# Performance work log

Measured on AMD Instinct MI355X. Metric: run time of the kernel, lower is better.

The kernel has to match this reference:

```python
import jax, jax.numpy as jnp
import numpy as np

B, C, H, W = 64, 256, 14, 14
K = 9
HID = 256   # EdgeAgg hidden_channels = in_channels
OUT = 512   # out_channels = 2*in_channels (required by final reshape)


def _knn(q, kset, k):
    # ViG dense_knn_matrix: squared-distance knn, top-k of -dist (self-loop may be included)
    qs = jnp.sum(q * q, -1)
    ks = jnp.sum(kset * kset, -1)
    dist = qs[:, :, None] - 2.0 * jnp.einsum('bnc,bmc->bnm', q, kset) + ks[:, None, :]
    _, idx = jax.lax.top_k(-dist, k)   # (B,N,k) neighbor indices into kset
    return idx


def _edgeconv_add(feat, nbr, validf, w, b):
    # PyG EdgeConv(nn=Linear, aggr='add') with per-node valid-edge mask:
    #   out[i] = sum_{j in valid nbrs(i)} cat(x_i, x_j - x_i) @ w + b
    # nn is linear, so aggregate neighbor diffs BEFORE the matmul (same math, less traffic).
    Cf = feat.shape[-1]
    wa, wb = w[:Cf], w[Cf:]
    deg = jnp.sum(validf, -1, keepdims=True)                   # (B,N,1)
    xj = feat[jnp.arange(feat.shape[0])[:, None, None], nbr]   # (B,N,k,C) gather
    sum_xj = jnp.einsum('bnkc,bnk->bnc', xj, validf)
    return deg * (feat @ wa + b) + (sum_xj - deg * feat) @ wb


def _forward(x, fc1_w, fc1_b, fc2_w, fc2_b, fce_w, fce_b, inout_w, inout_b,
             attn_w, attn_b, upd_w, upd_b, kp_w, kp_b, enc_w, enc_b,
             mu_w, mu_b, dec_w, dec_b, T):
    k = dec_w.shape[-1]
    b_, c_, h_, w_ = x.shape
    n = h_ * w_
    xs = x.reshape(b_, c_, n)                       # (B,C,N)
    x_sp = jnp.transpose(xs, (0, 2, 1))             # (B,N,C) true spatial node feats for knn
    x_sp_d = jax.lax.stop_gradient(x_sp)            # original detaches before knn
    x_nbr = _knn(x_sp_d, x_sp_d, k)
    # temporal roll across the T frames of each clip
    y_sp = jnp.roll(x_sp.reshape(b_ // T, T, n, c_), -1, axis=1).reshape(b_, n, c_)
    y_nbr = _knn(x_sp_d, jax.lax.stop_gradient(y_sp), k)
    # faithful to original: x.view(B*N, C) reinterprets the contiguous (B,C,N) buffer
    x_feat = xs.reshape(b_, n, c_)
    y_feat = jnp.transpose(y_sp, (0, 2, 1)).reshape(b_, n, c_)
    # VAE-like K predictor (deterministic z = mu); argmax -> per-node degree in [0,k)
    hk = x_feat.reshape(b_ * n, c_) @ kp_w + kp_b
    hk = jax.nn.relu(hk @ enc_w + enc_b)
    mu = hk @ mu_w + mu_b
    logits = mu @ dec_w + dec_b                     # (B*N, k)
    k_int = jnp.argmax(logits, axis=1)
    # generate_mask: keep the first k_int[i] of node i's k edges
    validf = (jnp.arange(k)[None, :] < k_int[:, None]).astype(x.dtype).reshape(b_, n, k)

    def edge_agg(feat, nbr):
        h1 = jax.nn.relu(_edgeconv_add(feat, nbr, validf, fc1_w, fc1_b))
        h2 = _edgeconv_add(h1, nbr, validf, fc2_w, fc2_b)
        return (h2 @ fce_w + fce_b).reshape(b_ * n, -1)

    x_agg = edge_agg(x_feat, x_nbr)
    y_agg = edge_agg(y_feat, y_nbr)
    scores = (jnp.concatenate([x_agg, y_agg], -1) @ attn_w + attn_b)[:, 0]
    wgt = jax.nn.softmax(scores, axis=0)[:, None]   # softmax over ALL B*N nodes (as in source)
    fused = wgt * x_agg + (1.0 - wgt) * y_agg
    xin = x_feat.reshape(b_ * n, c_) @ inout_w + inout_b
    upd = jax.nn.relu(jnp.concatenate([xin, fused], -1) @ upd_w + upd_b)   # (B*N, 2C)
    return jnp.transpose(upd.reshape(b_, n, 2 * c_), (0, 2, 1)).reshape(b_, 2 * c_, h_, w_)


def setup_inputs():
    key = jax.random.key(0)
    ks = iter(jax.random.split(key, 32))

    def lin(i, o):
        return jax.random.normal(next(ks), (i, o), jnp.float32) / np.sqrt(i)

    def bias(o):
        return jax.random.normal(next(ks), (o,), jnp.float32) * 0.01

    return {
        'x': jax.random.normal(next(ks), (B, C, H, W), jnp.float32),
        'fc1_w': lin(2 * C, HID), 'fc1_b': bias(HID),
        'fc2_w': lin(2 * HID, HID), 'fc2_b': bias(HID),
        'fce_w': lin(HID, OUT), 'fce_b': bias(OUT),
        'inout_w': lin(C, OUT), 'inout_b': bias(OUT),
        'attn_w': lin(2 * OUT, 1), 'attn_b': bias(1),
        'upd_w': lin(2 * OUT, OUT), 'upd_b': bias(OUT),
        'kp_w': lin(C, 500), 'kp_b': bias(500),
        'enc_w': lin(500, 64), 'enc_b': bias(64),
        'mu_w': lin(64, 32), 'mu_b': bias(32),
        'dec_w': lin(32, K), 'dec_b': bias(K),
        'T': 16,
    }


def reference(x, fc1_w, fc1_b, fc2_w, fc2_b, fce_w, fce_b, inout_w, inout_b,
              attn_w, attn_b, upd_w, upd_b, kp_w, kp_b, enc_w, enc_b,
              mu_w, mu_b, dec_w, dec_b, T):
    return _forward(x, fc1_w, fc1_b, fc2_w, fc2_b, fce_w, fce_b, inout_w, inout_b,
                    attn_w, attn_b, upd_w, upd_b, kp_w, kp_b, enc_w, enc_b,
                    mu_w, mu_b, dec_w, dec_b, T)
```

## Files before the change

### kernel.cpp

```cpp
#include <hip/hip_runtime.h>
#include <cstddef>
#include <cstdint>

constexpr int BATCH = 64;
constexpr int CH    = 256;
constexpr int NPT   = 196;
constexpr int ROWS  = BATCH * NPT;
constexpr int BSTRIDE = CH * NPT;
constexpr int KNB   = 8;
constexpr int DSTR  = 208;

typedef __bf16 bf16x8 __attribute__((ext_vector_type(8)));
typedef __bf16 bf16x4 __attribute__((ext_vector_type(4)));
typedef _Float16 f16x8 __attribute__((ext_vector_type(8)));
typedef float  f32x4  __attribute__((ext_vector_type(4)));
typedef unsigned long long u64;

__device__ __forceinline__ int src_batch(int b) {
    return (b & ~15) | ((b + 1) & 15);
}

__device__ __forceinline__ void gload_lds16(const void* g, void* l) {
    __builtin_amdgcn_global_load_lds(
        (const __attribute__((address_space(1))) void*)g,
        (__attribute__((address_space(3))) void*)l, 16, 0, 0);
}

__device__ __forceinline__ int xcd_swz(int lin, int nwg) {
    int q = nwg >> 3;
    return (lin & 7) * q + (lin >> 3);
}

__global__ __launch_bounds__(256) void front_kernel(const float* __restrict__ x,
        _Float16* __restrict__ XH, _Float16* __restrict__ XL,
        __bf16* __restrict__ XB, float* __restrict__ qsp,
        const float* __restrict__ fc1_w, const float* __restrict__ fc2_w,
        const float* __restrict__ fce_w, const float* __restrict__ upd_w,
        const float* __restrict__ kp_w, const float* __restrict__ kp_b,
        const float* __restrict__ enc_w, const float* __restrict__ enc_b,
        const float* __restrict__ mu_w, const float* __restrict__ mu_b,
        const float* __restrict__ dec_w, const float* __restrict__ dec_b,
        const float* __restrict__ inout_w, const float* __restrict__ inout_b,
        const float* __restrict__ upd_b,
        __bf16* __restrict__ W1catT, __bf16* __restrict__ W2catT,
        __bf16* __restrict__ fcet, __bf16* __restrict__ updC,
        float* __restrict__ KW1, float* __restrict__ kb1,
        float* __restrict__ KW2, float* __restrict__ kb2,
        float* __restrict__ bcomp, int* __restrict__ smcnt) {
    __shared__ __attribute__((aligned(16))) char smem[16896];
    float (*tile)[65] = (float(*)[65])smem;
    int bid = blockIdx.x;
    int t = threadIdx.x;
    if (bid < 1024) {
        int m0 = (bid & 3) * 64, c0 = ((bid >> 2) & 3) * 64, b = bid >> 4;
        const float* xb = x + (size_t)b * BSTRIDE;
        #pragma unroll
        for (int s = 0; s < 16; ++s) {
            int idx = s * 256 + t;
            int cc = idx >> 6, mm = idx & 63;
            int m = m0 + mm;
            float v = (m < NPT) ? xb[(size_t)(c0 + cc) * NPT + m] : 0.f;
            tile[cc][mm] = v;
            if (m < NPT)
                XB[(size_t)b * BSTRIDE + (size_t)(c0 + cc) * NPT + m] = (__bf16)v;
        }
        __syncthreads();
        #pragma unroll
        for (int s = 0; s < 16; ++s) {
            int idx = s * 256 + t;
            int mm = idx >> 6, cc = idx & 63;
            float v = tile[cc][mm];
            _Float16 h = (_Float16)v;
            size_t off = ((size_t)b * 256 + (m0 + mm)) * 256 + c0 + cc;
            XH[off] = h;
            XL[off] = (_Float16)(v - (float)h);
        }
        if (t < 64) {
            float acc = 0.f;
            #pragma unroll
            for (int cc = 0; cc < 64; ++cc) {
                float v = tile[cc][t];
                acc = fmaf(v, v, acc);
            }
            qsp[(size_t)(c0 >> 6) * 16384 + b * 256 + m0 + t] = acc;
        }
    } else {
        int pbid = bid - 1024;
        if (pbid == 0 && t == 0) smcnt[0] = 0;
        if (pbid < 64) {
            const float* W = (pbid < 32) ? fc1_w : fc2_w;
            __bf16* WT = (pbid < 32) ? W1catT : W2catT;
            int local = pbid & 31;
            int n0 = (local >> 2) * 64, k0 = (local & 3) * 64;
            #pragma unroll
            for (int s = 0; s < 16; ++s) {
                int idx = s * 256 + t;
                int kk = idx >> 6, nn = idx & 63;
                float v;
                if (n0 < 256)
                    v = W[(size_t)(k0 + kk) * 256 + n0 + nn] -
                        W[(size_t)(k0 + kk + 256) * 256 + n0 + nn];
                else
                    v = W[(size_t)(k0 + kk + 256) * 256 + (n0 - 256) + nn];
                tile[kk][nn] = v;
            }
            __syncthreads();
            #pragma unroll
            for (int s = 0; s < 16; ++s) {
                int idx = s * 256 + t;
                int nn = idx >> 6, kk = idx & 63;
                WT[(size_t)(n0 + nn) * 256 + k0 + kk] = (__bf16)tile[kk][nn];
            }
        } else if (pbid < 96) {
            int local = pbid - 64;
            int n0 = (local >> 2) * 64, k0 = (local & 3) * 64;
            #pragma unroll
            for (int s = 0; s < 16; ++s) {
                int idx = s * 256 + t;
                int kk = idx >> 6, nn = idx & 63;
                tile[kk][nn] = fce_w[(size_t)(k0 + kk) * 512 + n0 + nn];
            }
            __syncthreads();
            #pragma unroll
            for (int s = 0; s < 16; ++s) {
                int idx = s * 256 + t;
                int nn = idx >> 6, kk = idx & 63;
                fcet[(size_t)(n0 + nn) * 256 + k0 + kk] = (__bf16)tile[kk][nn];
            }
        } else if (pbid < 160) {
            int local = pbid - 96;
            int k0 = (local >> 3) * 64, n0 = (local & 7) * 64;
            #pragma unroll
            for (int s = 0; s < 16; ++s) {
                int idx = s * 256 + t;
                int kk = idx >> 6, nn = idx & 63;
                tile[kk][nn] = upd_w[(size_t)(512 + k0 + kk) * 512 + n0 + nn];
            }
            __syncthreads();
            #pragma unroll
            for (int s = 0; s < 16; ++s) {
                int idx = s * 256 + t;
                int nn = idx >> 6, kk = idx & 63;
                updC[(size_t)(n0 + nn) * 768 + 256 + k0 + kk] = (__bf16)tile[kk][nn];
            }
        } else if (pbid < 224) {
            int i = (pbid - 160) * 4 + (t >> 6);
            int j = t & 63;
            double acc = 0.0;
            for (int k = 0; k < 500; ++k)
                acc += (double)kp_w[(size_t)i * 500 + k] * (double)enc_w[(size_t)k * 64 + j];
            KW1[i * 64 + j] = (float)acc;
        } else if (pbid == 224) {
            int j = t;
            if (j < 64) {
                double acc = (double)enc_b[j];
                for (int k = 0; k < 500; ++k)
                    acc += (double)kp_b[k] * (double)enc_w[(size_t)k * 64 + j];
                kb1[j] = (float)acc;
            }
        } else if (pbid < 228) {
            int e = (pbid - 225) * 256 + t;
            if (e < 576) {
                int i = e / 9, j = e - (e / 9) * 9;
                double acc = 0.0;
                for (int k = 0; k < 32; ++k)
                    acc += (double)mu_w[(size_t)i * 32 + k] * (double)dec_w[(size_t)k * 9 + j];
                KW2[e] = (float)acc;
            } else if (e < 585) {
                int j = e - 576;
                double acc = (double)dec_b[j];
                for (int k = 0; k < 32; ++k)
                    acc += (double)mu_b[k] * (double)dec_w[(size_t)k * 9 + j];
                kb2[j] = (float)acc;
            }
        } else if (pbid < 740) {
            int e = (pbid - 228) * 256 + t;
            int k = e >> 9, n = e & 511;
            double acc = 0.0;
            for (int j = 0; j < 512; ++j)
                acc += (double)inout_w[(size_t)k * 512 + j] * (double)upd_w[(size_t)j * 512 + n];
            updC[(size_t)n * 768 + k] = (__bf16)(float)acc;
        } else {
            int n = (pbid - 740) * 256 + t;
            double acc = (double)upd_b[n];
            for (int j = 0; j < 512; ++j)
                acc += (double)inout_b[j] * (double)upd_w[(size_t)j * 512 + n];
            bcomp[n] = (float)acc;
        }
    }
}

__global__ __launch_bounds__(256) void gram_kint(const _Float16* __restrict__ XH,
        const _Float16* __restrict__ XL, const float* __restrict__ qsp,
        float* __restrict__ Dw, const float* __restrict__ x,
        const float* __restrict__ W1, const float* __restrict__ b1,
        const float* __restrict__ W2, const float* __restrict__ b2,
        int* __restrict__ kint, float* __restrict__ degf) {
    __shared__ __attribute__((aligned(16))) char smem[32768];
    int bid = blockIdx.x;
    int t = threadIdx.x;
    if (bid < 2048) {
        int nid = xcd_swz(bid, 2048);
        int job = nid >> 4;
        int tile = nid & 15;
        int by = tile >> 2, bx = tile & 3;
        int r0 = by * 64, c0 = bx * 64;
        int qb = (job < 64) ? job : job - 64;
        int kb = (job < 64) ? qb : src_batch(qb);
        int w = t >> 6, l = t & 63;
        int lr = l & 15, lg = l >> 4;
        int wr = (w >> 1) * 32, wc = (w & 1) * 32;
        const _Float16* qh = XH + (size_t)qb * 65536;
        const _Float16* ql = XL + (size_t)qb * 65536;
        const _Float16* kh = XH + (size_t)kb * 65536;
        const _Float16* kl = XL + (size_t)kb * 65536;
        int srow = w * 16 + (l >> 2);
        int scb = (l & 3) * 8;
        f32x4 acc[2][2] = {};
        auto stage = [&](int k0, int bsel) {
            _Float16* base = (_Float16*)(smem + bsel * 16384);
            size_t goA = (size_t)(r0 + srow) * 256 + k0 + scb;
            size_t goB = (size_t)(c0 + srow) * 256 + k0 + scb;
            gload_lds16(qh + goA, base + w * 512);
            gload_lds16(ql + goA, base + 2048 + w * 512);
            gload_lds16(kh + goB, base + 4096 + w * 512);
            gload_lds16(kl + goB, base + 6144 + w * 512);
        };
        stage(0, 0);
        #pragma unroll
        for (int ks8 = 0; ks8 < 8; ++ks8) {
            if (ks8 < 7) {
                stage((ks8 + 1) * 32, (ks8 + 1) & 1);
                asm volatile("s_waitcnt vmcnt(4)" ::: "memory");
            } else {
                asm volatile("s_waitcnt vmcnt(0)" ::: "memory");
            }
            __syncthreads();
            _Float16* base = (_Float16*)(smem + (ks8 & 1) * 16384);
            _Float16* Ah = base;
            _Float16* Al = base + 2048;
            _Float16* Bh = base + 4096;
            _Float16* Bl = base + 6144;
            f16x8 ah[2], alv[2], bh[2], blv[2];
            #pragma unroll
            for (int mi = 0; mi < 2; ++mi) {
                ah[mi]  = *(const f16x8*)(Ah + (wr + mi * 16 + lr) * 32 + lg * 8);
                alv[mi] = *(const f16x8*)(Al + (wr + mi * 16 + lr) * 32 + lg * 8);
            }
            #pragma unroll
            for (int ni = 0; ni < 2; ++ni) {
                bh[ni]  = *(const f16x8*)(Bh + (wc + ni * 16 + lr) * 32 + lg * 8);
                blv[ni] = *(const f16x8*)(Bl + (wc + ni * 16 + lr) * 32 + lg * 8);
            }
            #pragma unroll
            for (int mi = 0; mi < 2; ++mi)
                #pragma unroll
                for (int ni = 0; ni < 2; ++ni) {
                    acc[mi][ni] = __builtin_amdgcn_mfma_f32_16x16x32_f16(
                        ah[mi], bh[ni], acc[mi][ni], 0, 0, 0);
                    acc[mi][ni] = __builtin_amdgcn_mfma_f32_16x16x32_f16(
                        ah[mi], blv[ni], acc[mi][ni], 0, 0, 0);
                    acc[mi][ni] = __builtin_amdgcn_mfma_f32_16x16x32_f16(
                        alv[mi], bh[ni], acc[mi][ni], 0, 0, 0);
                }
            __syncthreads();
        }
        float ksv[2];
        #pragma unroll
        for (int ni = 0; ni < 2; ++ni) {
            int col = c0 + wc + ni * 16 + lr;
            if (col < NPT) {
                size_t o0 = (size_t)kb * 256 + col;
                ksv[ni] = ((qsp[o0] + qsp[16384 + o0]) + qsp[32768 + o0]) +
                          qsp[49152 + o0];
            } else ksv[ni] = 0.f;
        }
        #pragma unroll
        for (int mi = 0; mi < 2; ++mi) {
            #pragma unroll
            for (int r = 0; r < 4; ++r) {
                if (r0 + wr + mi * 16 + r >= NPT) continue;
                int grow = r0 + wr + mi * 16 + lg * 4 + r;
                if (grow >= NPT) continue;
                size_t o0 = (size_t)qb * 256 + grow;
                float qq = ((qsp[o0] + qsp[16384 + o0]) + qsp[32768 + o0]) +
                           qsp[49152 + o0];
                size_t rbase = ((size_t)job * NPT + grow) * DSTR;
                #pragma unroll
                for (int ni = 0; ni < 2; ++ni) {
                    int col = c0 + wc + ni * 16 + lr;
                    if (col < NPT)
                        Dw[rbase + col] = qq - 2.f * acc[mi][ni][r] + ksv[ni];
                }
            }
        }
    } else {
        float (*xr)[256] = (float(*)[256])smem;
        float (*ebuf)[64] = (float(*)[64])(smem + 16384);
        float (*lg2)[9]  = (float(*)[9])(smem + 20480);
        int r0 = (bid - 2048) * 16;
        const float4* xg = (const float4*)(x + (size_t)r0 * 256);
        float4* xs = (float4*)&xr[0][0];
        #pragma unroll
        for (int s = 0; s < 4; ++s) xs[s * 256 + t] = xg[s * 256 + t];
        __syncthreads();
        int w = t >> 6, l = t & 63;
        {
            float bb = b1[l];
            float a0 = bb, a1 = bb, a2 = bb, a3 = bb;
            const float* x0 = xr[w * 4 + 0];
            const float* x1 = xr[w * 4 + 1];
            const float* x2 = xr[w * 4 + 2];
            const float* x3 = xr[w * 4 + 3];
            for (int c = 0; c < 256; ++c) {
                float wv = W1[c * 64 + l];
                a0 = fmaf(x0[c], wv, a0);
                a1 = fmaf(x1[c], wv, a1);
                a2 = fmaf(x2[c], wv, a2);
                a3 = fmaf(x3[c], wv, a3);
            }
            ebuf[w * 4 + 0][l] = fmaxf(a0, 0.f);
            ebuf[w * 4 + 1][l] = fmaxf(a1, 0.f);
            ebuf[w * 4 + 2][l] = fmaxf(a2, 0.f);
            ebuf[w * 4 + 3][l] = fmaxf(a3, 0.f);
        }
        __syncthreads();
        int rr = t >> 4, cc = t & 15;
        if (cc < 9) {
            float acc = b2[cc];
            for (int j = 0; j < 64; ++j)
                acc = fmaf(ebuf[rr][j], W2[j * 9 + cc], acc);
            lg2[rr][cc] = acc;
        }
        __syncthreads();
        if (cc == 0) {
            float best = lg2[rr][0];
            int bi = 0;
            #pragma unroll
            for (int j = 1; j < 9; ++j)
                if (lg2[rr][j] > best) { best = lg2[rr][j]; bi = j; }
            kint[r0 + rr] = bi;
            degf[r0 + rr] = (float)bi;
        }
    }
}

__global__ __launch_bounds__(256) void topk_p1(const float* __restrict__ Dw,
        int* __restrict__ nbr, const __bf16* __restrict__ XB,
        const __bf16* __restrict__ W1catT, __bf16* __restrict__ P1) {
    __shared__ __attribute__((aligned(16))) char smem[32768];
    int bid = blockIdx.x;
    int t = threadIdx.x;
    if (bid < 392) {
        u64 (*lists)[4][8] = (u64(*)[4][8])smem;
        int lrow = t >> 2, q = t & 3;
        int rowid = bid * 64 + lrow;
        const float* rp = Dw + (size_t)rowid * DSTR + q * 52;
        u64 kreg[8];
        #pragma unroll
        for (int p = 0; p < 8; ++p) kreg[p] = ~0ull;
        for (int s4 = 0; s4 < 13; ++s4) {
            f32x4 dv = *(const f32x4*)(rp + s4 * 4);
            #pragma unroll
            for (int e = 0; e < 4; ++e) {
                int col = q * 52 + s4 * 4 + e;
                unsigned u = __float_as_uint(dv[e]);
                u = (u & 0x80000000u) ? ~u : (u | 0x80000000u);
                u64 key = (col < NPT) ? (((u64)u << 32) | (unsigned)col) : ~0ull;
                if (key < kreg[7]) {
                    #pragma unroll
                    for (int p = 0; p < 8; ++p) {
                        u64 mn = (key < kreg[p]) ? key : kreg[p];
                        u64 mx = (key < kreg[p]) ? kreg[p] : key;
                        kreg[p] = mn; key = mx;
                    }
                }
            }
        }
        #pragma unroll
        for (int p = 0; p < 8; ++p) lists[lrow][q][p] = kreg[p];
        __syncthreads();
        if (q == 0) {
            const u64* c = &lists[lrow][0][0];
            int p0 = 0, p1 = 0, p2 = 0, p3 = 0;
            #pragma unroll
            for (int it = 0; it < 8; ++it) {
                u64 v0 = c[p0], v1 = c[8 + p1], v2 = c[16 + p2], v3 = c[24 + p3];
                u64 best = v0; int bj = 0;
                if (v1 < best) { best = v1; bj = 1; }
                if (v2 < best) { best = v2; bj = 2; }
                if (v3 < best) { best = v3; bj = 3; }
                if (bj == 0) p0 = (p0 < 7) ? p0 + 1 : 7;
                else if (bj == 1) p1 = (p1 < 7) ? p1 + 1 : 7;
                else if (bj == 2) p2 = (p2 < 7) ? p2 + 1 : 7;
                else p3 = (p3 < 7) ? p3 + 1 : 7;
                nbr[(size_t)rowid * KNB + it] = (int)(best & 0xffffffffu);
            }
        }
    } else {
        __bf16* As = (__bf16*)smem;
        __bf16* Bs = As + 128 * 64;
        int lin = bid - 392;
        int nid = xcd_swz(lin, 392);
        int bx = nid & 3, by = nid >> 2;
        int w = t >> 6, l = t & 63;
        int r0 = by * 128, c0 = bx * 128;
        int lr = l & 15, lg = l >> 4;
        int wr = (w >> 1) * 64, wc = (w & 1) * 64;
        constexpr int K = 256, N = 512;
        f32x4 acc[4][4] = {};
        for (int k0 = 0; k0 < K; k0 += 64) {
            #pragma unroll
            for (int i = 0; i < 4; ++i) {
                int row = (w * 4 + i) * 8 + (l >> 3);
                int c8 = l & 7;
                gload_lds16(XB + (size_t)(r0 + row) * K + k0 + c8 * 8,
                            As + (w * 4 + i) * 512);
                gload_lds16(W1catT + (size_t)(c0 + row) * K + k0 + c8 * 8,
                            Bs + (w * 4 + i) * 512);
            }
            asm volatile("s_waitcnt vmcnt(0)" ::: "memory");
            __syncthreads();
            #pragma unroll
            for (int ks = 0; ks < 2; ++ks) {
                bf16x8 af[4], bfr[4];
                #pragma unroll
                for (int mi = 0; mi < 4; ++mi)
                    af[mi] = *(const bf16x8*)(As + (wr + mi * 16 + lr) * 64 + ks * 32 + lg * 8);
                #pragma unroll
                for (int ni = 0; ni < 4; ++ni)
                    bfr[ni] = *(const bf16x8*)(Bs + (wc + ni * 16 + lr) * 64 + ks * 32 + lg * 8);
                #pragma unroll
                for (int mi = 0; mi < 4; ++mi)
                    #pragma unroll
                    for (int ni = 0; ni < 4; ++ni)
                        acc[mi][ni] = __builtin_amdgcn_mfma_f32_16x16x32_bf16(
                            af[mi], bfr[ni], acc[mi][ni], 0, 0, 0);
            }
            __syncthreads();
        }
        #pragma unroll
        for (int mi = 0; mi < 4; ++mi) {
            #pragma unroll
            for (int r = 0; r < 4; ++r) {
                int row = r0 + wr + mi * 16 + lg * 4 + r;
                #pragma unroll
                for (int ni = 0; ni < 4; ++ni) {
                    int col = c0 + wc + ni * 16 + lr;
                    P1[(size_t)row * N + col] = (__bf16)acc[mi][ni][r];
                }
            }
        }
    }
}

template<int STAGE, int RELU>
__global__ __launch_bounds__(256) void combine_kernel(const __bf16* __restrict__ P,
        const int* __restrict__ nbr, const int* __restrict__ kint_,
        const float* __restrict__ degf, const float* __restrict__ bias,
        __bf16* __restrict__ H) {
    int g = threadIdx.x >> 6, lane = threadIdx.x & 63;
    int nid = xcd_swz(blockIdx.x, 2 * ROWS / 4);
    int r = nid * 4 + g;
    int branch = (r >= ROWS);
    int rr = r - branch * ROWS;
    int b = rr / NPT, i = rr - b * NPT;
    size_t srow, mbase;
    if constexpr (STAGE == 1) {
        int fb = branch ? src_batch(b) : b;
        srow = (size_t)fb * NPT + i;
        mbase = (size_t)fb * NPT;
    } else {
        srow = (size_t)r;
        mbase = (size_t)branch * ROWS + (size_t)b * NPT;
    }
    const int* nb = nbr + (size_t)branch * ((size_t)ROWS * KNB) + (size_t)rr * KNB;
    bf16x4 sv = *(const bf16x4*)(P + srow * 512 + lane * 4);
    float4 bv = *(const float4*)(bias + lane * 4);
    float s0 = 0.f, s1 = 0.f, s2 = 0.f, s3 = 0.f;
    int kk = kint_[rr];
    for (int tt = 0; tt < kk; ++tt) {
        int m = nb[tt];
        bf16x4 v = *(const bf16x4*)(P + (mbase + m) * 512 + 256 + lane * 4);
        s0 += (float)v[0]; s1 += (float)v[1]; s2 += (float)v[2]; s3 += (float)v[3];
    }
    float dg = degf[rr];
    float o0 = fmaf(dg, (float)sv[0] + bv.x, s0);
    float o1 = fmaf(dg, (float)sv[1] + bv.y, s1);
    float o2 = fmaf(dg, (float)sv[2] + bv.z, s2);
    float o3 = fmaf(dg, (float)sv[3] + bv.w, s3);
    if constexpr (RELU) {
        o0 = fmaxf(o0, 0.f); o1 = fmaxf(o1, 0.f);
        o2 = fmaxf(o2, 0.f); o3 = fmaxf(o3, 0.f);
    }
    bf16x4 ov;
    ov[0] = (__bf16)o0; ov[1] = (__bf16)o1; ov[2] = (__bf16)o2; ov[3] = (__bf16)o3;
    *(bf16x4*)(H + (size_t)r * 256 + lane * 4) = ov;
}

template<int FLAGS, int CONCAT>
__global__ __launch_bounds__(256) void mfma_gemm(
    const __bf16* __restrict__ A0, const __bf16* __restrict__ A1,
    const __bf16* __restrict__ WT, const float* __restrict__ bias,
    float* __restrict__ Cf, __bf16* __restrict__ Cb, int K, int N,
    const float* __restrict__ aw, float* __restrict__ scp,
    const float* __restrict__ wgt) {
    constexpr int SMEMB = (FLAGS & 8) ? (128 * 129 * 4) : (2 * 128 * 64 * 2);
    __shared__ __attribute__((aligned(16))) char smem[SMEMB];
    __bf16* As = (__bf16*)smem;
    __bf16* Bs = As + 128 * 64;
    int lin = blockIdx.x + 4 * blockIdx.y;
    int nid = xcd_swz(lin, 4 * gridDim.y);
    int bx = nid & 3, by = nid >> 2;
    int t = threadIdx.x, w = t >> 6, l = t & 63;
    int r0 = by * 128, c0 = bx * 128;
    int lr = l & 15, lg = l >> 4;
    int wr = (w >> 1) * 64, wc = (w & 1) * 64;
    f32x4 acc[4][4] = {};
    for (int k0 = 0; k0 < K; k0 += 64) {
        #pragma unroll
        for (int i = 0; i < 4; ++i) {
            int row = (w * 4 + i) * 8 + (l >> 3);
            int c8 = l & 7;
            if constexpr (CONCAT == 2) {
                if (k0 < 256) {
                    gload_lds16(A0 + (size_t)(r0 + row) * 256 + k0 + c8 * 8,
                                As + (w * 4 + i) * 512);
                } else {
                    int kk2 = k0 - 256 + c8 * 8;
                    size_t gr = (size_t)(r0 + row);
                    bf16x8 xa = *(const bf16x8*)(A1 + gr * 512 + kk2);
                    bf16x8 ya = *(const bf16x8*)(A1 + ((size_t)ROWS + gr) * 512 + kk2);
                    float wv = wgt[gr];
                    bf16x8 mx;
                    #pragma unroll
                    for (int j = 0; j < 8; ++j)
                        mx[j] = (__bf16)(wv * (float)xa[j] + (1.f - wv) * (float)ya[j]);
                    *(bf16x8*)(As + (w * 4 + i) * 512 + l * 8) = mx;
                }
            } else {
                gload_lds16(A0 + (size_t)(r0 + row) * K + k0 + c8 * 8,
                            As + (w * 4 + i) * 512);
            }
            gload_lds16(WT + (size_t)(c0 + row) * K + k0 + c8 * 8,
                        Bs + (w * 4 + i) * 512);
        }
        asm volatile("s_waitcnt vmcnt(0)" ::: "memory");
        __syncthreads();
        #pragma unroll
        for (int ks = 0; ks < 2; ++ks) {
            bf16x8 af[4], bfr[4];
            #pragma unroll
            for (int mi = 0; mi < 4; ++mi)
                af[mi] = *(const bf16x8*)(As + (wr + mi * 16 + lr) * 64 + ks * 32 + lg * 8);
            #pragma unroll
            for (int ni = 0; ni < 4; ++ni)
                bfr[ni] = *(const bf16x8*)(Bs + (wc + ni * 16 + lr) * 64 + ks * 32 + lg * 8);
            #pragma unroll
            for (int mi = 0; mi < 4; ++mi)
                #pragma unroll
                for (int ni = 0; ni < 4; ++ni)
                    acc[mi][ni] = __builtin_amdgcn_mfma_f32_16x16x32_bf16(
                        af[mi], bfr[ni], acc[mi][ni], 0, 0, 0);
        }
        __syncthreads();
    }
    if constexpr ((FLAGS & 8) != 0) {
        float* tile = (float*)smem;
        #pragma unroll
        for (int mi = 0; mi < 4; ++mi)
            #pragma unroll
            for (int r = 0; r < 4; ++r) {
                int rrow = wr + mi * 16 + lg * 4 + r;
                #pragma unroll
                for (int ni = 0; ni < 4; ++ni) {
                    int ccol = wc + ni * 16 + lr;
                    float v = acc[mi][ni][r];
                    if (bias) v += bias[c0 + ccol];
                    if constexpr ((FLAGS & 1) != 0) v = fmaxf(v, 0.f);
                    tile[rrow * 129 + ccol] = v;
                }
            }
        __syncthreads();
        int cc = t >> 6, rr2 = t & 63;
        #pragma unroll
        for (int cs = 0; cs < 128; cs += 4) {
            #pragma unroll
            for (int h = 0; h < 2; ++h) {
                int row = r0 + rr2 + h * 64;
                int bb = row / NPT, ii = row - bb * NPT;
                Cf[((size_t)bb * 512 + (c0 + cc + cs)) * NPT + ii] =
                    tile[(rr2 + h * 64) * 129 + cc + cs];
            }
        }
    } else if constexpr ((FLAGS & 16) != 0) {
        int half = (r0 >= ROWS) ? 1 : 0;
        float ps[4][4] = {};
        #pragma unroll
        for (int mi = 0; mi < 4; ++mi)
            #pragma unroll
            for (int r = 0; r < 4; ++r) {
                int row = r0 + wr + mi * 16 + lg * 4 + r;
                #pragma unroll
                for (int ni = 0; ni < 4; ++ni) {
                    int col = c0 + wc + ni * 16 + lr;
                    float v = acc[mi][ni][r] + bias[col];
                    Cb[(size_t)row * N + col] = (__bf16)v;
                    ps[mi][r] = fmaf(v, aw[half * 512 + col], ps[mi][r]);
                }
            }
        #pragma unroll
        for (int m = 1; m <= 8; m <<= 1)
            #pragma unroll
            for (int mi = 0; mi < 4; ++mi)
                #pragma unroll
                for (int r = 0; r < 4; ++r)
                    ps[mi][r] += __shfl_xor(ps[mi][r], m, 64);
        if (lr == 0) {
            int slot = half * 8 + bx * 2 + (w & 1);
            #pragma unroll
            for (int mi = 0; mi < 4; ++mi)
                #pragma unroll
                for (int r = 0; r < 4; ++r) {
                    int sr = r0 - half * ROWS + wr + mi * 16 + lg * 4 + r;
                    scp[(size_t)slot * ROWS + sr] = ps[mi][r];
                }
        }
    } else {
        #pragma unroll
        for (int mi = 0; mi < 4; ++mi) {
            #pragma unroll
            for (int r = 0; r < 4; ++r) {
                int row = r0 + wr + mi * 16 + lg * 4 + r;
                #pragma unroll
                for (int ni = 0; ni < 4; ++ni) {
                    int col = c0 + wc + ni * 16 + lr;
                    float v = acc[mi][ni][r];
                    if (bias) v += bias[col];
                    if constexpr ((FLAGS & 1) != 0) v = fmaxf(v, 0.f);
                    if constexpr ((FLAGS & 4) != 0)
                        Cb[(size_t)row * N + col] = (__bf16)v;
                    else
                        Cf[(size_t)row * N + col] = v;
                }
            }
        }
    }
}

__global__ __launch_bounds__(256) void softmax_all(const float* __restrict__ scp,
        const float* __restrict__ ab, float* __restrict__ scores,
        float* __restrict__ mpart, float* __restrict__ spart,
        int* __restrict__ cnt, float* __restrict__ wgt) {
    __shared__ float red[256];
    __shared__ float MS[2];
    __shared__ bool islast;
    int t = threadIdx.x;
    int sr = blockIdx.x * 256 + t;
    float s = ab[0];
    #pragma unroll
    for (int i = 0; i < 16; ++i) s += scp[(size_t)i * ROWS + sr];
    scores[sr] = s;
    red[t] = s; __syncthreads();
    for (int off = 128; off; off >>= 1) {
        if (t < off) red[t] = fmaxf(red[t], red[t + off]);
        __syncthreads();
    }
    float mb = red[0]; __syncthreads();
    red[t] = expf(s - mb); __syncthreads();
    for (int off = 128; off; off >>= 1) {
        if (t < off) red[t] += red[t + off];
        __syncthreads();
    }
    if (t == 0) {
        mpart[blockIdx.x] = mb;
        spart[blockIdx.x] = red[0];
        __threadfence();
        int old = atomicAdd(cnt, 1);
        islast = (old == 48);
    }
    __syncthreads();
    if (!islast) return;
    __threadfence();
    if (t == 0) {
        float M = mpart[0];
        for (int i = 1; i < 49; ++i) M = fmaxf(M, mpart[i]);
        float S = 0.f;
        for (int i = 0; i < 49; ++i) S += spart[i] * expf(mpart[i] - M);
        MS[0] = M; MS[1] = S;
        cnt[0] = 0;
    }
    __syncthreads();
    float M = MS[0], denom = MS[1];
    for (int i = t; i < ROWS; i += 256)
        wgt[i] = expf(scores[i] - M) / denom;
}

extern "C" void kernel_launch(void* const* d_in, const int* in_sizes, int n_in,
                              void* d_out, int out_size, void* d_ws, size_t ws_size,
                              hipStream_t stream) {
    (void)in_sizes; (void)n_in; (void)out_size; (void)ws_size;
    const float* x       = (const float*)d_in[0];
    const float* fc1_w   = (const float*)d_in[1];
    const float* fc1_b   = (const float*)d_in[2];
    const float* fc2_w   = (const float*)d_in[3];
    const float* fc2_b   = (const float*)d_in[4];
    const float* fce_w   = (const float*)d_in[5];
    const float* fce_b   = (const float*)d_in[6];
    const float* inout_w = (const float*)d_in[7];
    const float* inout_b = (const float*)d_in[8];
    const float* attn_w  = (const float*)d_in[9];
    const float* attn_b  = (const float*)d_in[10];
    const float* upd_w   = (const float*)d_in[11];
    const float* upd_b   = (const float*)d_in[12];
    const float* kp_w    = (const float*)d_in[13];
    const float* kp_b    = (const float*)d_in[14];
    const float* enc_w   = (const float*)d_in[15];
    const float* enc_b   = (const float*)d_in[16];
    const float* mu_w    = (const float*)d_in[17];
    const float* mu_b    = (const float*)d_in[18];
    const float* dec_w   = (const float*)d_in[19];
    const float* dec_b   = (const float*)d_in[20];
    float* out = (float*)d_out;

    char* base = (char*)d_ws;
    size_t o = 0;
    auto alloc = [&](size_t bytes) -> void* {
        void* p = base + o;
        o += (bytes + 255) & ~(size_t)255;
        return p;
    };
    float* qsp    = (float*)alloc((size_t)4 * 64 * 256 * 4);
    float* degf   = (float*)alloc(ROWS * 4);
    float* scores = (float*)alloc(ROWS * 4);
    float* wgt    = (float*)alloc(ROWS * 4);
    int*   kint   = (int*)  alloc(ROWS * 4);
    float* KW1    = (float*)alloc(256 * 64 * 4);
    float* kb1    = (float*)alloc(64 * 4);
    float* KW2    = (float*)alloc(64 * 9 * 4);
    float* kb2    = (float*)alloc(9 * 4);
    float* bcomp  = (float*)alloc(512 * 4);
    float* scp    = (float*)alloc((size_t)16 * ROWS * 4);
    float* mpart  = (float*)alloc(64 * 4);
    float* spart  = (float*)alloc(64 * 4);
    int*   smcnt  = (int*)  alloc(256);
    int*   nbr    = (int*)  alloc((size_t)128 * NPT * KNB * 4);
    char*  regD   = (char*) alloc((size_t)ROWS * 512 * 2);
    __bf16* XB    = (__bf16*)alloc((size_t)ROWS * 256 * 2);
    __bf16* H1    = (__bf16*)alloc((size_t)2 * ROWS * 256 * 2);
    __bf16* H2    = (__bf16*)alloc((size_t)2 * ROWS * 256 * 2);
    char*  regAGG = (char*) alloc((size_t)2 * ROWS * 512 * 4);
    __bf16* W1catT= (__bf16*)alloc((size_t)512 * 256 * 2);
    __bf16* W2catT= (__bf16*)alloc((size_t)512 * 256 * 2);
    __bf16* fcet  = (__bf16*)alloc((size_t)512 * 256 * 2);
    __bf16* updC  = (__bf16*)alloc((size_t)512 * 768 * 2);
    __bf16* P1buf = (__bf16*)regD;
    _Float16* XSPH = (_Float16*)regAGG;
    _Float16* XSPL = XSPH + (size_t)64 * 256 * 256;
    float* Dw     = (float*)(regAGG + (size_t)17 * 1024 * 1024);
    __bf16* P2buf = (__bf16*)regAGG;
    __bf16* AGGb  = (__bf16*)regAGG;
    __bf16* XAGGb = AGGb;

    front_kernel<<<1766, 256, 0, stream>>>(x, XSPH, XSPL, XB, qsp,
                                           fc1_w, fc2_w, fce_w, upd_w,
                                           kp_w, kp_b, enc_w, enc_b,
                                           mu_w, mu_b, dec_w, dec_b,
                                           inout_w, inout_b, upd_b,
                                           W1catT, W2catT, fcet, updC,
                                           KW1, kb1, KW2, kb2, bcomp, smcnt);

    gram_kint<<<2832, 256, 0, stream>>>(XSPH, XSPL, qsp, Dw, x,
                                        KW1, kb1, KW2, kb2, kint, degf);

    topk_p1<<<784, 256, 0, stream>>>(Dw, nbr, XB, W1catT, P1buf);

    combine_kernel<1, 1><<<2 * ROWS / 4, 256, 0, stream>>>(
        P1buf, nbr, kint, degf, fc1_b, H1);

    mfma_gemm<4, 0><<<dim3(4, 196), 256, 0, stream>>>(
        H1, nullptr, W2catT, nullptr, nullptr, P2buf, 256, 512,
        nullptr, nullptr, nullptr);
    combine_kernel<2, 0><<<2 * ROWS / 4, 256, 0, stream>>>(
        P2buf, nbr, kint, degf, fc2_b, H2);

    mfma_gemm<20, 0><<<dim3(4, 196), 256, 0, stream>>>(
        H2, nullptr, fcet, fce_b, nullptr, AGGb, 256, 512,
        attn_w, scp, nullptr);

    softmax_all<<<49, 256, 0, stream>>>(scp, attn_b, scores, mpart, spart,
                                        smcnt, wgt);

    mfma_gemm<9, 2><<<dim3(4, 98), 256, 0, stream>>>(
        XB, XAGGb, updC, bcomp, out, nullptr, 768, 512,
        nullptr, nullptr, wgt);
}
```

Baseline: 210.7 us.

## Move later-stage weight prep from front kernel into topk kernel blocks

The fc2, fce and upd weight transposes, the fp64 inout·upd weight fold and the bias fold now run as extra blocks of the top-k/P1 kernel instead of the front kernel. Only the fc1 transpose and the K-predictor weight folds stay in the front kernel. This shortens the front kernel, which sits on the critical path before the gram kernel, and lets the weight prep overlap with top-k work whose results are not needed until later stages. In exchange the top-k launch grows and its tail may lengthen, especially from the slow fp64 512-length dot-product blocks.

```diff
diff --git a/kernel.cpp b/kernel.cpp
--- a/kernel.cpp
+++ b/kernel.cpp
@@ -34,19 +34,15 @@
 __global__ __launch_bounds__(256) void front_kernel(const float* __restrict__ x,
         _Float16* __restrict__ XH, _Float16* __restrict__ XL,
         __bf16* __restrict__ XB, float* __restrict__ qsp,
-        const float* __restrict__ fc1_w, const float* __restrict__ fc2_w,
-        const float* __restrict__ fce_w, const float* __restrict__ upd_w,
+        const float* __restrict__ fc1_w,
         const float* __restrict__ kp_w, const float* __restrict__ kp_b,
         const float* __restrict__ enc_w, const float* __restrict__ enc_b,
         const float* __restrict__ mu_w, const float* __restrict__ mu_b,
         const float* __restrict__ dec_w, const float* __restrict__ dec_b,
-        const float* __restrict__ inout_w, const float* __restrict__ inout_b,
-        const float* __restrict__ upd_b,
-        __bf16* __restrict__ W1catT, __bf16* __restrict__ W2catT,
-        __bf16* __restrict__ fcet, __bf16* __restrict__ updC,
+        __bf16* __restrict__ W1catT,
         float* __restrict__ KW1, float* __restrict__ kb1,
         float* __restrict__ KW2, float* __restrict__ kb2,
-        float* __restrict__ bcomp, int* __restrict__ smcnt) {
+        int* __restrict__ smcnt) {
     __shared__ __attribute__((aligned(16))) char smem[16896];
     float (*tile)[65] = (float(*)[65])smem;
     int bid = blockIdx.x;
@@ -84,73 +80,17 @@
             }
             qsp[(size_t)(c0 >> 6) * 16384 + b * 256 + m0 + t] = acc;
         }
-    } else {
+    } else if (bid < 1092) {
         int pbid = bid - 1024;
         if (pbid == 0 && t == 0) smcnt[0] = 0;
         if (pbid < 64) {
-            const float* W = (pbid < 32) ? fc1_w : fc2_w;
-            __bf16* WT = (pbid < 32) ? W1catT : W2catT;
-            int local = pbid & 31;
-            int n0 = (local >> 2) * 64, k0 = (local & 3) * 64;
-            #pragma unroll
-            for (int s = 0; s < 16; ++s) {
-                int idx = s * 256 + t;
-                int kk = idx >> 6, nn = idx & 63;
-                float v;
-                if (n0 < 256)
-                    v = W[(size_t)(k0 + kk) * 256 + n0 + nn] -
-                        W[(size_t)(k0 + kk + 256) * 256 + n0 + nn];
-                else
-                    v = W[(size_t)(k0 + kk + 256) * 256 + (n0 - 256) + nn];
-                tile[kk][nn] = v;
-            }
-            __syncthreads();
-            #pragma unroll
-            for (int s = 0; s < 16; ++s) {
-                int idx = s * 256 + t;
-                int nn = idx >> 6, kk = idx & 63;
-                WT[(size_t)(n0 + nn) * 256 + k0 + kk] = (__bf16)tile[kk][nn];
-            }
-        } else if (pbid < 96) {
-            int local = pbid - 64;
-            int n0 = (local >> 2) * 64, k0 = (local & 3) * 64;
-            #pragma unroll
-            for (int s = 0; s < 16; ++s) {
-                int idx = s * 256 + t;
-                int kk = idx >> 6, nn = idx & 63;
-                tile[kk][nn] = fce_w[(size_t)(k0 + kk) * 512 + n0 + nn];
-            }
-            __syncthreads();
-            #pragma unroll
-            for (int s = 0; s < 16; ++s) {
-                int idx = s * 256 + t;
-                int nn = idx >> 6, kk = idx & 63;
-                fcet[(size_t)(n0 + nn) * 256 + k0 + kk] = (__bf16)tile[kk][nn];
-            }
-        } else if (pbid < 160) {
-            int local = pbid - 96;
-            int k0 = (local >> 3) * 64, n0 = (local & 7) * 64;
-            #pragma unroll
-            for (int s = 0; s < 16; ++s) {
-                int idx = s * 256 + t;
-                int kk = idx >> 6, nn = idx & 63;
-                tile[kk][nn] = upd_w[(size_t)(512 + k0 + kk) * 512 + n0 + nn];
-            }
-            __syncthreads();
-            #pragma unroll
-            for (int s = 0; s < 16; ++s) {
-                int idx = s * 256 + t;
-                int nn = idx >> 6, kk = idx & 63;
-                updC[(size_t)(n0 + nn) * 768 + 256 + k0 + kk] = (__bf16)tile[kk][nn];
-            }
-        } else if (pbid < 224) {
-            int i = (pbid - 160) * 4 + (t >> 6);
+            int i = pbid * 4 + (t >> 6);
             int j = t & 63;
             double acc = 0.0;
             for (int k = 0; k < 500; ++k)
                 acc += (double)kp_w[(size_t)i * 500 + k] * (double)enc_w[(size_t)k * 64 + j];
             KW1[i * 64 + j] = (float)acc;
-        } else if (pbid == 224) {
+        } else if (pbid == 64) {
             int j = t;
             if (j < 64) {
                 double acc = (double)enc_b[j];
@@ -158,8 +98,8 @@
                     acc += (double)kp_b[k] * (double)enc_w[(size_t)k * 64 + j];
                 kb1[j] = (float)acc;
             }
-        } else if (pbid < 228) {
-            int e = (pbid - 225) * 256 + t;
+        } else {
+            int e = (pbid - 65) * 256 + t;
             if (e < 576) {
                 int i = e / 9, j = e - (e / 9) * 9;
                 double acc = 0.0;
@@ -173,19 +113,28 @@
                     acc += (double)mu_b[k] * (double)dec_w[(size_t)k * 9 + j];
                 kb2[j] = (float)acc;
             }
-        } else if (pbid < 740) {
-            int e = (pbid - 228) * 256 + t;
-            int k = e >> 9, n = e & 511;
-            double acc = 0.0;
-            for (int j = 0; j < 512; ++j)
-                acc += (double)inout_w[(size_t)k * 512 + j] * (double)upd_w[(size_t)j * 512 + n];
-            updC[(size_t)n * 768 + k] = (__bf16)(float)acc;
-        } else {
-            int n = (pbid - 740) * 256 + t;
-            double acc = (double)upd_b[n];
-            for (int j = 0; j < 512; ++j)
-                acc += (double)inout_b[j] * (double)upd_w[(size_t)j * 512 + n];
-            bcomp[n] = (float)acc;
+        }
+    } else {
+        int local = bid - 1092;
+        int n0 = (local >> 2) * 64, k0 = (local & 3) * 64;
+        #pragma unroll
+        for (int s = 0; s < 16; ++s) {
+            int idx = s * 256 + t;
+            int kk = idx >> 6, nn = idx & 63;
+            float v;
+            if (n0 < 256)
+                v = fc1_w[(size_t)(k0 + kk) * 256 + n0 + nn] -
+                    fc1_w[(size_t)(k0 + kk + 256) * 256 + n0 + nn];
+            else
+                v = fc1_w[(size_t)(k0 + kk + 256) * 256 + (n0 - 256) + nn];
+            tile[kk][nn] = v;
+        }
+        __syncthreads();
+        #pragma unroll
+        for (int s = 0; s < 16; ++s) {
+            int idx = s * 256 + t;
+            int nn = idx >> 6, kk = idx & 63;
+            W1catT[(size_t)(n0 + nn) * 256 + k0 + kk] = (__bf16)tile[kk][nn];
         }
     }
 }
@@ -347,7 +296,12 @@
 
 __global__ __launch_bounds__(256) void topk_p1(const float* __restrict__ Dw,
         int* __restrict__ nbr, const __bf16* __restrict__ XB,
-        const __bf16* __restrict__ W1catT, __bf16* __restrict__ P1) {
+        const __bf16* __restrict__ W1catT, __bf16* __restrict__ P1,
+        const float* __restrict__ fc2_w, const float* __restrict__ fce_w,
+        const float* __restrict__ upd_w, const float* __restrict__ inout_w,
+        const float* __restrict__ inout_b, const float* __restrict__ upd_b,
+        __bf16* __restrict__ W2catT, __bf16* __restrict__ fcet,
+        __bf16* __restrict__ updC, float* __restrict__ bcomp) {
     __shared__ __attribute__((aligned(16))) char smem[32768];
     int bid = blockIdx.x;
     int t = threadIdx.x;
@@ -397,7 +351,7 @@
                 nbr[(size_t)rowid * KNB + it] = (int)(best & 0xffffffffu);
             }
         }
-    } else {
+    } else if (bid < 784) {
         __bf16* As = (__bf16*)smem;
         __bf16* Bs = As + 128 * 64;
         int lin = bid - 392;
@@ -451,6 +405,76 @@
                 }
             }
         }
+    } else if (bid < 816) {
+        float (*tile)[65] = (float(*)[65])smem;
+        int local = bid - 784;
+        int n0 = (local >> 2) * 64, k0 = (local & 3) * 64;
+        #pragma unroll
+        for (int s = 0; s < 16; ++s) {
+            int idx = s * 256 + t;
+            int kk = idx >> 6, nn = idx & 63;
+            float v;
+            if (n0 < 256)
+                v = fc2_w[(size_t)(k0 + kk) * 256 + n0 + nn] -
+                    fc2_w[(size_t)(k0 + kk + 256) * 256 + n0 + nn];
+            else
+                v = fc2_w[(size_t)(k0 + kk + 256) * 256 + (n0 - 256) + nn];
+            tile[kk][nn] = v;
+        }
+        __syncthreads();
+        #pragma unroll
+        for (int s = 0; s < 16; ++s) {
+            int idx = s * 256 + t;
+            int nn = idx >> 6, kk = idx & 63;
+            W2catT[(size_t)(n0 + nn) * 256 + k0 + kk] = (__bf16)tile[kk][nn];
+        }
+    } else if (bid < 848) {
+        float (*tile)[65] = (float(*)[65])smem;
+        int local = bid - 816;
+        int n0 = (local >> 2) * 64, k0 = (local & 3) * 64;
+        #pragma unroll
+        for (int s = 0; s < 16; ++s) {
+            int idx = s * 256 + t;
+            int kk = idx >> 6, nn = idx & 63;
+            tile[kk][nn] = fce_w[(size_t)(k0 + kk) * 512 + n0 + nn];
+        }
+        __syncthreads();
+        #pragma unroll
+        for (int s = 0; s < 16; ++s) {
+            int idx = s * 256 + t;
+            int nn = idx >> 6, kk = idx & 63;
+            fcet[(size_t)(n0 + nn) * 256 + k0 + kk] = (__bf16)tile[kk][nn];
+        }
+    } else if (bid < 912) {
+        float (*tile)[65] = (float(*)[65])smem;
+        int local = bid - 848;
+        int k0 = (local >> 3) * 64, n0 = (local & 7) * 64;
+        #pragma unroll
+        for (int s = 0; s < 16; ++s) {
+            int idx = s * 256 + t;
+            int kk = idx >> 6, nn = idx & 63;
+            tile[kk][nn] = upd_w[(size_t)(512 + k0 + kk) * 512 + n0 + nn];
+        }
+        __syncthreads();
+        #pragma unroll
+        for (int s = 0; s < 16; ++s) {
+            int idx = s * 256 + t;
+            int nn = idx >> 6, kk = idx & 63;
+            updC[(size_t)(n0 + nn) * 768 + 256 + k0 + kk] = (__bf16)tile[kk][nn];
+        }
+    } else if (bid < 1424) {
+        int e = (bid - 912) * 256 + t;
+        int k = e >> 9, n = e & 511;
+        double acc = 0.0;
+        for (int j = 0; j < 512; ++j)
+            acc += (double)inout_w[(size_t)k * 512 + j] * (double)upd_w[(size_t)j * 512 + n];
+        updC[(size_t)n * 768 + k] = (__bf16)(float)acc;
+    } else {
+        int n = (bid - 1424) * 256 + t;
+        double acc = (double)upd_b[n];
+        for (int j = 0; j < 512; ++j)
+            acc += (double)inout_b[j] * (double)upd_w[(size_t)j * 512 + n];
+        bcomp[n] = (float)acc;
     }
 }
 
@@ -762,18 +786,18 @@
     __bf16* AGGb  = (__bf16*)regAGG;
     __bf16* XAGGb = AGGb;
 
-    front_kernel<<<1766, 256, 0, stream>>>(x, XSPH, XSPL, XB, qsp,
-                                           fc1_w, fc2_w, fce_w, upd_w,
-                                           kp_w, kp_b, enc_w, enc_b,
+    front_kernel<<<1124, 256, 0, stream>>>(x, XSPH, XSPL, XB, qsp,
+                                           fc1_w, kp_w, kp_b, enc_w, enc_b,
                                            mu_w, mu_b, dec_w, dec_b,
-                                           inout_w, inout_b, upd_b,
-                                           W1catT, W2catT, fcet, updC,
-                                           KW1, kb1, KW2, kb2, bcomp, smcnt);
+                                           W1catT, KW1, kb1, KW2, kb2, smcnt);
 
     gram_kint<<<2832, 256, 0, stream>>>(XSPH, XSPL, qsp, Dw, x,
                                         KW1, kb1, KW2, kb2, kint, degf);
 
-    topk_p1<<<784, 256, 0, stream>>>(Dw, nbr, XB, W1catT, P1buf);
+    topk_p1<<<1426, 256, 0, stream>>>(Dw, nbr, XB, W1catT, P1buf,
+                                      fc2_w, fce_w, upd_w, inout_w,
+                                      inout_b, upd_b,
+                                      W2catT, fcet, updC, bcomp);
 
     combine_kernel<1, 1><<<2 * ROWS / 4, 256, 0, stream>>>(
         P1buf, nbr, kint, degf, fc1_b, H1);
```

Result: slower. 224.1 us (+6.3%).
